# Kernel optimization log

Hardware: AMD Instinct MI355X
Metric: run time of the kernel (lower is better)

## Reference

```python
import jax, jax.numpy as jnp
import numpy as np

EPS = 1e-5
KS = 3
PAD = 1


def _bn(x, g, b, m, v):
    inv = g / jnp.sqrt(v + EPS)
    return x * inv[None, :, None, None] + (b - m * inv)[None, :, None, None]


def _deform_conv2d(x, off_w, off_b, w):
    # x: (B,C,H,W); off_w: (2*9,C,3,3); w: (Cout,C,3,3)
    B, C, H, W = x.shape
    N = KS * KS
    off = jax.lax.conv_general_dilated(x, off_w, (1, 1), ((PAD, PAD), (PAD, PAD)))
    off = off + off_b[None, :, None, None]                      # (B,2N,H,W)
    xp = jnp.pad(x, ((0, 0), (0, 0), (PAD, PAD), (PAD, PAD)))
    Hp, Wp = H + 2 * PAD, W + 2 * PAD
    r = jnp.arange(KS, dtype=x.dtype) - (KS - 1) // 2           # kernel offsets
    pny = jnp.repeat(r, KS)                                     # row-major (dy)
    pnx = jnp.tile(r, KS)                                       # row-major (dx)
    p0y = jnp.arange(1, H + 1, dtype=x.dtype)[None, None, :, None]
    p0x = jnp.arange(1, W + 1, dtype=x.dtype)[None, None, None, :]
    py = off[:, :N] + pny[None, :, None, None] + p0y            # (B,N,H,W)
    px = off[:, N:] + pnx[None, :, None, None] + p0x
    py = jnp.clip(py, 0.0, Hp - 1.0)
    px = jnp.clip(px, 0.0, Wp - 1.0)
    fy = jax.lax.stop_gradient(jnp.floor(py))                   # indices detached (as in torch impl)
    fx = jax.lax.stop_gradient(jnp.floor(px))
    qy0 = jnp.clip(fy, 0.0, Hp - 1.0)
    qx0 = jnp.clip(fx, 0.0, Wp - 1.0)
    qy1 = jnp.clip(fy + 1.0, 0.0, Hp - 1.0)
    qx1 = jnp.clip(fx + 1.0, 0.0, Wp - 1.0)
    xf = xp.reshape(B, C, Hp * Wp)

    def gather(qy, qx):
        idx = (qy * Wp + qx).astype(jnp.int32)                  # (B,N,H,W)
        return jax.vmap(lambda m_, i_: m_[:, i_])(xf, idx)       # (B,C,N,H,W)

    g_lt = (1.0 + (qy0 - py)) * (1.0 + (qx0 - px))
    g_rb = (1.0 - (qy1 - py)) * (1.0 - (qx1 - px))
    g_lb = (1.0 + (qy0 - py)) * (1.0 - (qx1 - px))
    g_rt = (1.0 - (qy1 - py)) * (1.0 + (qx0 - px))
    xo = (g_lt[:, None] * gather(qy0, qx0) + g_rb[:, None] * gather(qy1, qx1)
          + g_lb[:, None] * gather(qy0, qx1) + g_rt[:, None] * gather(qy1, qx0))
    # (B,C,N,H,W) -> (B,C,H*KS,W*KS): N = (row, col) row-major
    xo = xo.reshape(B, C, KS, KS, H, W).transpose(0, 1, 4, 2, 5, 3).reshape(B, C, H * KS, W * KS)
    return jax.lax.conv_general_dilated(xo, w, (KS, KS), 'VALID')


def _forward(x, dc1_offw, dc1_offb, dc1_w, bn1_g, bn1_b, bn1_m, bn1_v,
             dc2_offw, dc2_offb, dc2_w, bn2_g, bn2_b, bn2_m, bn2_v,
             id_w, id_b, bn3_g, bn3_b, bn3_m, bn3_v):
    h = jax.nn.relu(_bn(_deform_conv2d(x, dc1_offw, dc1_offb, dc1_w), bn1_g, bn1_b, bn1_m, bn1_v))
    h = _bn(_deform_conv2d(h, dc2_offw, dc2_offb, dc2_w), bn2_g, bn2_b, bn2_m, bn2_v)
    idt = jnp.einsum('bchw,oc->bohw', x, id_w[:, :, 0, 0]) + id_b[None, :, None, None]
    idt = _bn(idt, bn3_g, bn3_b, bn3_m, bn3_v)
    return jax.nn.relu(h + idt)


def setup_inputs() -> dict:
    key = jax.random.key(0)
    ks = jax.random.split(key, 16)
    B, Cin, Cout, H, W = 2, 64, 128, 128, 128
    N2 = 2 * KS * KS
    d = {}
    d['x'] = jax.random.normal(ks[0], (B, Cin, H, W), jnp.float32)
    d['dc1_offw'] = jax.random.normal(ks[1], (N2, Cin, KS, KS), jnp.float32) * 0.01
    d['dc1_offb'] = jnp.zeros((N2,), jnp.float32)
    d['dc1_w'] = jax.random.normal(ks[2], (Cout, Cin, KS, KS), jnp.float32) * 0.05
    d['bn1_g'] = 1.0 + 0.1 * jax.random.normal(ks[3], (Cout,), jnp.float32)
    d['bn1_b'] = 0.1 * jax.random.normal(ks[4], (Cout,), jnp.float32)
    d['bn1_m'] = 0.1 * jax.random.normal(ks[5], (Cout,), jnp.float32)
    d['bn1_v'] = jnp.ones((Cout,), jnp.float32)
    d['dc2_offw'] = jax.random.normal(ks[6], (N2, Cout, KS, KS), jnp.float32) * 0.01
    d['dc2_offb'] = jnp.zeros((N2,), jnp.float32)
    d['dc2_w'] = jax.random.normal(ks[7], (Cout, Cout, KS, KS), jnp.float32) * 0.03
    d['bn2_g'] = 1.0 + 0.1 * jax.random.normal(ks[8], (Cout,), jnp.float32)
    d['bn2_b'] = 0.1 * jax.random.normal(ks[9], (Cout,), jnp.float32)
    d['bn2_m'] = 0.1 * jax.random.normal(ks[10], (Cout,), jnp.float32)
    d['bn2_v'] = jnp.ones((Cout,), jnp.float32)
    d['id_w'] = jax.random.normal(ks[11], (Cout, Cin, 1, 1), jnp.float32) * 0.1
    d['id_b'] = jnp.zeros((Cout,), jnp.float32)
    d['bn3_g'] = 1.0 + 0.1 * jax.random.normal(ks[12], (Cout,), jnp.float32)
    d['bn3_b'] = 0.1 * jax.random.normal(ks[13], (Cout,), jnp.float32)
    d['bn3_m'] = 0.1 * jax.random.normal(ks[14], (Cout,), jnp.float32)
    d['bn3_v'] = jnp.ones((Cout,), jnp.float32)
    return d


def reference(x, dc1_offw, dc1_offb, dc1_w, bn1_g, bn1_b, bn1_m, bn1_v,
              dc2_offw, dc2_offb, dc2_w, bn2_g, bn2_b, bn2_m, bn2_v,
              id_w, id_b, bn3_g, bn3_b, bn3_m, bn3_v):
    return _forward(x, dc1_offw, dc1_offb, dc1_w, bn1_g, bn1_b, bn1_m, bn1_v,
                    dc2_offw, dc2_offb, dc2_w, bn2_g, bn2_b, bn2_m, bn2_v,
                    id_w, id_b, bn3_g, bn3_b, bn3_m, bn3_v)
```

## Files before the change

kernel.cpp:

```cpp
#include <hip/hip_runtime.h>
#include <math.h>

#define HH 128
#define WW 128
#define HWSZ (HH * WW)
#define BB 2
#define COUT 128

typedef __bf16 bf16x8 __attribute__((ext_vector_type(8)));
typedef float f32x4 __attribute__((ext_vector_type(4)));
typedef float f32x2 __attribute__((ext_vector_type(2)));
typedef short s16x8 __attribute__((ext_vector_type(8)));
typedef short s16x4 __attribute__((ext_vector_type(4)));
typedef unsigned short u16x4 __attribute__((ext_vector_type(4)));
typedef unsigned short u16x8 __attribute__((ext_vector_type(8)));

__device__ __forceinline__ short tobf(float f) {
  union { float f; unsigned u; } v; v.f = f;
  unsigned r = v.u + 0x7fffu + ((v.u >> 16) & 1u);
  return (short)(r >> 16);
}
__device__ __forceinline__ float asf(unsigned u) {
  union { unsigned u; float f; } v; v.u = u;
  return v.f;
}
__device__ __forceinline__ f32x2 up2(unsigned u) {
  f32x2 r; r[0] = asf(u << 16); r[1] = asf(u & 0xffff0000u); return r;
}
__device__ __forceinline__ unsigned trunc2bf(f32x2 v) {
  union { float f; unsigned u; } a, b;
  a.f = v[0]; b.f = v[1];
  return __builtin_amdgcn_perm(b.u, a.u, 0x07060302u);
}

#define PA0 73728
#define PA1 221184
#define PA2 229376
#define PA3 247808
#define PA4 284672
#define PA5 284928
__global__ __launch_bounds__(256) void prep_all_kernel(
    const float* __restrict__ dc1_w, const float* __restrict__ dc2_w,
    const float* __restrict__ id_w, const float* __restrict__ dc1_offw,
    const float* __restrict__ dc2_offw,
    const float* g1, const float* b1, const float* m1, const float* v1,
    const float* g2, const float* b2, const float* m2, const float* v2,
    const float* g3, const float* b3, const float* m3, const float* v3,
    const float* idb,
    short* __restrict__ wbf1, short* __restrict__ wbf2,
    short* __restrict__ woff1, short* __restrict__ woff2,
    float* __restrict__ cb1, float* __restrict__ cb2) {
  int idx = blockIdx.x * 256 + threadIdx.x;
  if (idx < PA0) {
    int o = idx / 576, k = idx - o * 576;
    float inv = g1[o] / sqrtf(v1[o] + 1e-5f);
    int col = (k % 9) * 64 + k / 9;
    int di = (((col >> 5) * 2 + (o >> 6)) * 4 + ((o >> 4) & 3)) * 512
           + (((o & 15) | (((col >> 3) & 3) << 4)) * 8) + (col & 7);
    wbf1[di] = tobf(dc1_w[(size_t)o * 576 + k] * inv);
  } else if (idx < PA1) {
    int j = idx - PA0;
    int o = j / 1152, k = j - o * 1152;
    float inv = g2[o] / sqrtf(v2[o] + 1e-5f);
    int col = (k % 9) * 128 + k / 9;
    int di = (((col >> 5) * 2 + (o >> 6)) * 4 + ((o >> 4) & 3)) * 512
           + (((o & 15) | (((col >> 3) & 3) << 4)) * 8) + (col & 7);
    wbf2[di] = tobf(dc2_w[(size_t)o * 1152 + k] * inv);
  } else if (idx < PA2) {
    int j = idx - PA1;
    int o = j >> 6, k = j & 63;
    float inv = g3[o] / sqrtf(v3[o] + 1e-5f);
    int col = 1152 + k;
    int di = (((col >> 5) * 2 + (o >> 6)) * 4 + ((o >> 4) & 3)) * 512
           + (((o & 15) | (((col >> 3) & 3) << 4)) * 8) + (col & 7);
    wbf2[di] = tobf(id_w[(size_t)o * 64 + k] * inv);
  } else if (idx < PA3) {
    int j = idx - PA2;
    int o = j / 576, k = j - o * 576;
    int col = (k % 9) * 64 + k / 9;
    int di = ((col >> 5) * 2 + (o >> 4)) * 512 + ((col >> 3) & 3) * 128
           + (o & 15) * 8 + (col & 7);
    woff1[di] = (o < 18) ? tobf(dc1_offw[(size_t)o * 576 + k]) : (short)0;
  } else if (idx < PA4) {
    int j = idx - PA3;
    int o = j / 1152, k = j - o * 1152;
    int col = (k % 9) * 128 + k / 9;
    int di = ((col >> 5) * 2 + (o >> 4)) * 512 + ((col >> 3) & 3) * 128
           + (o & 15) * 8 + (col & 7);
    woff2[di] = (o < 18) ? tobf(dc2_offw[(size_t)o * 1152 + k]) : (short)0;
  } else if (idx < PA5) {
    int j = idx - PA4;
    if (j < 128) {
      float inv = g1[j] / sqrtf(v1[j] + 1e-5f);
      cb1[j] = b1[j] - m1[j] * inv;
    } else {
      int o = j - 128;
      float inv2_ = g2[o] / sqrtf(v2[o] + 1e-5f);
      float inv3_ = g3[o] / sqrtf(v3[o] + 1e-5f);
      cb2[o] = (b2[o] - m2[o] * inv2_) + idb[o] * inv3_ + (b3[o] - m3[o] * inv3_);
    }
  }
}

__global__ __launch_bounds__(256) void xcast_kernel(const float* __restrict__ x,
                                                    unsigned short* __restrict__ xn) {
  __shared__ short lds[64 * 72];
  int tid = threadIdx.x;
  int gp0 = blockIdx.x * 64;
  int b = gp0 >> 14;
  int pl0 = gp0 & 16383;
  int p = tid & 63;
  int cb = (tid >> 6) * 16;
#pragma unroll
  for (int i = 0; i < 16; i++) {
    int c = cb + i;
    lds[p * 72 + c] = tobf(x[((size_t)(b * 64 + c)) * HWSZ + pl0 + p]);
  }
  __syncthreads();
  int pw = tid >> 2, cseg = (tid & 3) * 16;
  u16x8 a = *(const u16x8*)&lds[pw * 72 + cseg];
  u16x8 b8 = *(const u16x8*)&lds[pw * 72 + cseg + 8];
  *(u16x8*)&xn[(size_t)(gp0 + pw) * 64 + cseg] = a;
  *(u16x8*)&xn[(size_t)(gp0 + pw) * 64 + cseg + 8] = b8;
}

__global__ __launch_bounds__(512, 4) void offconv_mfma_kernel(
    const unsigned short* __restrict__ in, const short* __restrict__ woff,
    const float* __restrict__ offb, float* __restrict__ off, int cshift) {
  __shared__ float redf[4 * 64 * 8];
  const int tid = threadIdx.x;
  const int lane = tid & 63, wv = tid >> 6;
  const int pxg = wv & 3, kh = wv >> 2;
  const int pb = ((blockIdx.x & 7) << 6) | (blockIdx.x >> 3);
  const int pix0 = pb << 6;
  const int x0 = pix0 & 127, y = (pix0 >> 7) & 127, b = pix0 >> 14;
  const int Cin = 1 << cshift;
  const int HK = (9 << cshift) >> 1;
  const int NCh = HK >> 5;
  const unsigned short* inb = in + (size_t)b * HWSZ * Cin;
  const int l15 = lane & 15, quad = lane >> 4;
  const int px = x0 + pxg * 16 + l15;

  f32x4 acc[2];
  acc[0] = (f32x4){0.f, 0.f, 0.f, 0.f};
  acc[1] = (f32x4){0.f, 0.f, 0.f, 0.f};

  for (int i = 0; i < NCh; i++) {
    int k0 = kh * HK + i * 32;
    int n = k0 >> cshift;
    int c0 = (k0 & (Cin - 1)) + quad * 8;
    int yy = y + n / 3 - 1;
    int xx = px + n % 3 - 1;
    bf16x8 bv = {};
    if (((unsigned)yy < (unsigned)HH) && ((unsigned)xx < (unsigned)WW))
      bv = *(const bf16x8*)&inb[((size_t)yy * WW + xx) * Cin + c0];
    int fbase = (k0 >> 5) * 1024 + lane * 8;
    bf16x8 a0 = *(const bf16x8*)&woff[fbase];
    bf16x8 a1 = *(const bf16x8*)&woff[fbase + 512];
    acc[0] = __builtin_amdgcn_mfma_f32_16x16x32_bf16(a0, bv, acc[0], 0, 0, 0);
    acc[1] = __builtin_amdgcn_mfma_f32_16x16x32_bf16(a1, bv, acc[1], 0, 0, 0);
  }
  if (kh == 1) {
    *(f32x4*)&redf[(pxg * 64 + lane) * 8] = acc[0];
    *(f32x4*)&redf[(pxg * 64 + lane) * 8 + 4] = acc[1];
  }
  __syncthreads();
  if (kh == 0) {
    acc[0] += *(const f32x4*)&redf[(pxg * 64 + lane) * 8];
    acc[1] += *(const f32x4*)&redf[(pxg * 64 + lane) * 8 + 4];
#pragma unroll
    for (int ot = 0; ot < 2; ot++) {
#pragma unroll
      for (int r = 0; r < 4; r++) {
        int o = ot * 16 + quad * 4 + r;
        if (o < 18)
          off[(size_t)(b * 18 + o) * HWSZ + y * WW + px] = acc[ot][r] + offb[o];
      }
    }
  }
}

template <int CSH, int KCONV, int KTOT, int MODE>
__global__ __launch_bounds__(256, 3) void deform_mfma_kernel(
    const unsigned short* __restrict__ in, const float* __restrict__ off,
    const short* __restrict__ wbf, const float* __restrict__ cbv,
    const unsigned short* __restrict__ xid, float* __restrict__ outf,
    unsigned short* __restrict__ outb) {
  __shared__ __align__(16) char smem[25088];
  uint4* dsu = (uint4*)smem;
  f32x4* redf = (f32x4*)smem;
  short* trans = (short*)(smem + 16384);

  const int tid = threadIdx.x;
  const int lane = tid & 63, wv = tid >> 6;
  const int pb = ((blockIdx.x & 7) << 7) | (blockIdx.x >> 3);
  const int pix0 = pb << 5;
  const int x0 = pix0 & 127, y = (pix0 >> 7) & 127, b = pix0 >> 14;
  const int Cin = 1 << CSH;
  const unsigned short* inb = in + (size_t)b * HWSZ * Cin;
  const int l15 = lane & 15, quad = lane >> 4;
  const int pxg = wv & 1, kh = wv >> 1;
  const int dp = pxg * 16 + (lane >> 2);
  const int cq = lane & 3;
  const int baddr = (((lane & 15) << 2) | (lane >> 4)) << 2;

  for (int t = tid; t < 288; t += 256) {
    int n = t >> 5, pp = t & 31;
    float offy = off[(size_t)(b * 18 + n) * HWSZ + y * WW + x0 + pp];
    float offx = off[(size_t)(b * 18 + 9 + n) * HWSZ + y * WW + x0 + pp];
    float py = offy + (float)(n / 3 - 1) + (float)(y + 1);
    float px = offx + (float)(n % 3 - 1) + (float)(x0 + pp + 1);
    py = fminf(fmaxf(py, 0.f), 129.f);
    px = fminf(fmaxf(px, 0.f), 129.f);
    float fy = floorf(py), fx = floorf(px);
    float qy1 = fminf(fy + 1.f, 129.f), qx1 = fminf(fx + 1.f, 129.f);
    float ty0 = 1.f + fy - py, ty1 = 1.f - (qy1 - py);
    float tx0 = 1.f + fx - px, tx1 = 1.f - (qx1 - px);
    int iy0 = (int)fy - 1, ix0 = (int)fx - 1;
    int iy1 = (int)qy1 - 1, ix1 = (int)qx1 - 1;
    if ((unsigned)iy0 >= (unsigned)HH) ty0 = 0.f;
    if ((unsigned)iy1 >= (unsigned)HH) ty1 = 0.f;
    if ((unsigned)ix0 >= (unsigned)WW) tx0 = 0.f;
    if ((unsigned)ix1 >= (unsigned)WW) tx1 = 0.f;
    int by0 = min(max(iy0, 0), HH - 1), by1 = min(max(iy1, 0), HH - 1);
    int bx0 = min(max(ix0, 0), WW - 1), bx1 = min(max(ix1, 0), WW - 1);
    uint4 d4;
    d4.x = (unsigned)(unsigned short)tobf(ty0 * tx0)
         | ((unsigned)(unsigned short)tobf(ty0 * tx1) << 16);
    d4.y = (unsigned)(unsigned short)tobf(ty1 * tx0)
         | ((unsigned)(unsigned short)tobf(ty1 * tx1) << 16);
    d4.z = (unsigned)((by0 * WW + bx0) * Cin);
    d4.w = (unsigned)((((by1 - by0) * WW * Cin) << 16) | ((bx1 - bx0) * Cin));
    dsu[t] = d4;
  }

  f32x4 acc[8];
#pragma unroll
  for (int j = 0; j < 8; j++) acc[j] = (f32x4){0.f, 0.f, 0.f, 0.f};

  __syncthreads();

  constexpr int NC = KTOT >> 5;
  constexpr int HC = NC >> 1;
  const short* wfb = wbf + lane * 8;

  for (int i = 0; i < HC; i++) {
    int kc = kh * HC + i;
    int k0 = kc << 5;
    const short* wf = wfb + (size_t)kc * 4096;
    bf16x8 a0 = *(const bf16x8*)(wf);
    bf16x8 a1 = *(const bf16x8*)(wf + 512);
    bf16x8 a2 = *(const bf16x8*)(wf + 1024);
    bf16x8 a3 = *(const bf16x8*)(wf + 1536);
    bf16x8 a4 = *(const bf16x8*)(wf + 2048);
    bf16x8 a5 = *(const bf16x8*)(wf + 2560);
    bf16x8 a6 = *(const bf16x8*)(wf + 3072);
    bf16x8 a7 = *(const bf16x8*)(wf + 3584);
    uint4 pk;
    if (k0 < KCONV) {
      int n = k0 >> CSH;
      int c0 = (k0 & (Cin - 1)) + cq * 8;
      uint4 d4 = dsu[(n << 5) + dp];
      int dx = (int)(d4.w & 0xffffu);
      int dy = (int)d4.w >> 16;
      const unsigned short* ptr = inb + (int)d4.z + c0;
      uint4 q00 = *(const uint4*)(ptr);
      uint4 q01 = *(const uint4*)(ptr + dx);
      uint4 q10 = *(const uint4*)(ptr + dy);
      uint4 q11 = *(const uint4*)(ptr + dx + dy);
      float w0 = asf(d4.x << 16), w1 = asf(d4.x & 0xffff0000u);
      float w2 = asf(d4.y << 16), w3 = asf(d4.y & 0xffff0000u);
      f32x2 v0 = up2(q00.x) * w0 + up2(q01.x) * w1 + up2(q10.x) * w2 + up2(q11.x) * w3;
      f32x2 v1 = up2(q00.y) * w0 + up2(q01.y) * w1 + up2(q10.y) * w2 + up2(q11.y) * w3;
      f32x2 v2 = up2(q00.z) * w0 + up2(q01.z) * w1 + up2(q10.z) * w2 + up2(q11.z) * w3;
      f32x2 v3 = up2(q00.w) * w0 + up2(q01.w) * w1 + up2(q10.w) * w2 + up2(q11.w) * w3;
      pk.x = trunc2bf(v0); pk.y = trunc2bf(v1);
      pk.z = trunc2bf(v2); pk.w = trunc2bf(v3);
    } else {
      int c = (k0 - KCONV) + cq * 8;
      pk = *(const uint4*)&xid[((size_t)(b * HWSZ) + y * WW + x0 + dp) * 64 + c];
    }
    union { int i[4]; bf16x8 v; } bu;
    bu.i[0] = __builtin_amdgcn_ds_bpermute(baddr, (int)pk.x);
    bu.i[1] = __builtin_amdgcn_ds_bpermute(baddr, (int)pk.y);
    bu.i[2] = __builtin_amdgcn_ds_bpermute(baddr, (int)pk.z);
    bu.i[3] = __builtin_amdgcn_ds_bpermute(baddr, (int)pk.w);
    bf16x8 bfr = bu.v;
    acc[0] = __builtin_amdgcn_mfma_f32_16x16x32_bf16(a0, bfr, acc[0], 0, 0, 0);
    acc[1] = __builtin_amdgcn_mfma_f32_16x16x32_bf16(a1, bfr, acc[1], 0, 0, 0);
    acc[2] = __builtin_amdgcn_mfma_f32_16x16x32_bf16(a2, bfr, acc[2], 0, 0, 0);
    acc[3] = __builtin_amdgcn_mfma_f32_16x16x32_bf16(a3, bfr, acc[3], 0, 0, 0);
    acc[4] = __builtin_amdgcn_mfma_f32_16x16x32_bf16(a4, bfr, acc[4], 0, 0, 0);
    acc[5] = __builtin_amdgcn_mfma_f32_16x16x32_bf16(a5, bfr, acc[5], 0, 0, 0);
    acc[6] = __builtin_amdgcn_mfma_f32_16x16x32_bf16(a6, bfr, acc[6], 0, 0, 0);
    acc[7] = __builtin_amdgcn_mfma_f32_16x16x32_bf16(a7, bfr, acc[7], 0, 0, 0);
  }

  __syncthreads();
  if (kh == 1) {
#pragma unroll
    for (int f = 0; f < 8; f++) redf[f * 128 + pxg * 64 + lane] = acc[f];
  }
  __syncthreads();
  if (kh == 0) {
#pragma unroll
    for (int f = 0; f < 8; f++) acc[f] += redf[f * 128 + pxg * 64 + lane];
    if (MODE == 1) {
#pragma unroll
      for (int f = 0; f < 8; f++) {
#pragma unroll
        for (int r = 0; r < 4; r++) {
          int o = (f >> 2) * 64 + (f & 3) * 16 + quad * 4 + r;
          outf[(size_t)(b * COUT + o) * HWSZ + y * WW + x0 + pxg * 16 + l15] =
              fmaxf(acc[f][r] + cbv[o], 0.f);
        }
      }
    } else {
      int pl = pxg * 16 + l15;
#pragma unroll
      for (int f = 0; f < 8; f++) {
        s16x4 t4;
#pragma unroll
        for (int r = 0; r < 4; r++) {
          int o = (f >> 2) * 64 + (f & 3) * 16 + quad * 4 + r;
          t4[r] = tobf(fmaxf(acc[f][r] + cbv[o], 0.f));
        }
        *(s16x4*)&trans[pl * 136 + (f >> 2) * 64 + (f & 3) * 16 + quad * 4] = t4;
      }
    }
  }
  if (MODE == 0) {
    __syncthreads();
    int pw = tid >> 3, cs = (tid & 7) * 16;
    u16x8 va = *(const u16x8*)&trans[pw * 136 + cs];
    u16x8 vb = *(const u16x8*)&trans[pw * 136 + cs + 8];
    size_t gb = ((size_t)(b * HWSZ) + y * WW + x0 + pw) * 128 + cs;
    *(u16x8*)&outb[gb] = va;
    *(u16x8*)&outb[gb + 8] = vb;
  }
}

extern "C" void kernel_launch(void* const* d_in, const int* in_sizes, int n_in,
                              void* d_out, int out_size, void* d_ws, size_t ws_size,
                              hipStream_t stream) {
  const float* x        = (const float*)d_in[0];
  const float* dc1_offw = (const float*)d_in[1];
  const float* dc1_offb = (const float*)d_in[2];
  const float* dc1_w    = (const float*)d_in[3];
  const float* bn1_g    = (const float*)d_in[4];
  const float* bn1_b    = (const float*)d_in[5];
  const float* bn1_m    = (const float*)d_in[6];
  const float* bn1_v    = (const float*)d_in[7];
  const float* dc2_offw = (const float*)d_in[8];
  const float* dc2_offb = (const float*)d_in[9];
  const float* dc2_w    = (const float*)d_in[10];
  const float* bn2_g    = (const float*)d_in[11];
  const float* bn2_b    = (const float*)d_in[12];
  const float* bn2_m    = (const float*)d_in[13];
  const float* bn2_v    = (const float*)d_in[14];
  const float* id_w     = (const float*)d_in[15];
  const float* id_b     = (const float*)d_in[16];
  const float* bn3_g    = (const float*)d_in[17];
  const float* bn3_b    = (const float*)d_in[18];
  const float* bn3_m    = (const float*)d_in[19];
  const float* bn3_v    = (const float*)d_in[20];

  float* wsf = (float*)d_ws;
  float* off1 = wsf;
  float* off2 = off1 + (size_t)BB * 18 * HWSZ;
  float* cb1  = off2 + (size_t)BB * 18 * HWSZ;
  float* cb2  = cb1 + 128;
  unsigned short* xbf = (unsigned short*)(cb2 + 128);
  unsigned short* h1  = xbf + (size_t)BB * HWSZ * 64;
  short* wbf1  = (short*)(h1 + (size_t)BB * HWSZ * COUT);
  short* wbf2  = wbf1 + (size_t)128 * 576;
  short* woff1 = wbf2 + (size_t)128 * 1216;
  short* woff2 = woff1 + (size_t)18 * 1024;

  hipLaunchKernelGGL(prep_all_kernel, dim3((PA5 + 255) / 256), dim3(256), 0, stream,
                     dc1_w, dc2_w, id_w, dc1_offw, dc2_offw,
                     bn1_g, bn1_b, bn1_m, bn1_v, bn2_g, bn2_b, bn2_m, bn2_v,
                     bn3_g, bn3_b, bn3_m, bn3_v, id_b,
                     wbf1, wbf2, woff1, woff2, cb1, cb2);
  hipLaunchKernelGGL(xcast_kernel, dim3(BB * HWSZ / 64), dim3(256), 0, stream, x, xbf);

  hipLaunchKernelGGL(offconv_mfma_kernel, dim3(512), dim3(512), 0, stream,
                     xbf, woff1, dc1_offb, off1, 6);
  hipLaunchKernelGGL((deform_mfma_kernel<6, 576, 576, 0>), dim3(1024), dim3(256), 0, stream,
                     xbf, off1, wbf1, cb1, (const unsigned short*)nullptr,
                     (float*)nullptr, h1);
  hipLaunchKernelGGL(offconv_mfma_kernel, dim3(512), dim3(512), 0, stream,
                     h1, woff2, dc2_offb, off2, 7);
  hipLaunchKernelGGL((deform_mfma_kernel<7, 1152, 1216, 1>), dim3(1024), dim3(256), 0, stream,
                     h1, off2, wbf2, cb2, xbf, (float*)d_out,
                     (unsigned short*)nullptr);
}
```

Measured before the change: 187.5 us.

## Software-pipeline deform conv gathers with double-buffered registers; template offset conv

The deform kernel's K loop now double-buffers weight fragments and bilinear gather loads in two register sets (A/B), so the loads for the next chunk are issued before the current chunk's interpolation and MFMAs run. The conv part and the identity part are split into separate loops, which removes the per-iteration branch. The offset conv kernel is templated on the channel shift so its loop count is a compile-time constant and can be fully unrolled. The extra register sets raise VGPR pressure under launch_bounds(256,3), which risks spills or lower occupancy.

```diff
diff --git a/kernel.cpp b/kernel.cpp
--- a/kernel.cpp
+++ b/kernel.cpp
@@ -124,19 +124,20 @@
   *(u16x8*)&xn[(size_t)(gp0 + pw) * 64 + cseg + 8] = b8;
 }
 
+template <int CSH>
 __global__ __launch_bounds__(512, 4) void offconv_mfma_kernel(
     const unsigned short* __restrict__ in, const short* __restrict__ woff,
-    const float* __restrict__ offb, float* __restrict__ off, int cshift) {
+    const float* __restrict__ offb, float* __restrict__ off) {
   __shared__ float redf[4 * 64 * 8];
+  constexpr int Cin = 1 << CSH;
+  constexpr int HK = (9 << CSH) >> 1;
+  constexpr int NCh = HK >> 5;
   const int tid = threadIdx.x;
   const int lane = tid & 63, wv = tid >> 6;
   const int pxg = wv & 3, kh = wv >> 2;
   const int pb = ((blockIdx.x & 7) << 6) | (blockIdx.x >> 3);
   const int pix0 = pb << 6;
   const int x0 = pix0 & 127, y = (pix0 >> 7) & 127, b = pix0 >> 14;
-  const int Cin = 1 << cshift;
-  const int HK = (9 << cshift) >> 1;
-  const int NCh = HK >> 5;
   const unsigned short* inb = in + (size_t)b * HWSZ * Cin;
   const int l15 = lane & 15, quad = lane >> 4;
   const int px = x0 + pxg * 16 + l15;
@@ -145,9 +146,10 @@
   acc[0] = (f32x4){0.f, 0.f, 0.f, 0.f};
   acc[1] = (f32x4){0.f, 0.f, 0.f, 0.f};
 
+#pragma unroll
   for (int i = 0; i < NCh; i++) {
     int k0 = kh * HK + i * 32;
-    int n = k0 >> cshift;
+    int n = k0 >> CSH;
     int c0 = (k0 & (Cin - 1)) + quad * 8;
     int yy = y + n / 3 - 1;
     int xx = px + n % 3 - 1;
@@ -180,6 +182,64 @@
   }
 }
 
+#define LOADW(P, kc_)                                           \
+  {                                                             \
+    const short* wf_ = wfb + (size_t)(kc_) * 4096;              \
+    P##w0 = *(const bf16x8*)(wf_);                              \
+    P##w1 = *(const bf16x8*)(wf_ + 512);                        \
+    P##w2 = *(const bf16x8*)(wf_ + 1024);                       \
+    P##w3 = *(const bf16x8*)(wf_ + 1536);                       \
+    P##w4 = *(const bf16x8*)(wf_ + 2048);                       \
+    P##w5 = *(const bf16x8*)(wf_ + 2560);                       \
+    P##w6 = *(const bf16x8*)(wf_ + 3072);                       \
+    P##w7 = *(const bf16x8*)(wf_ + 3584);                       \
+  }
+
+#define LOADT(P, kc_)                                           \
+  {                                                             \
+    int k0_ = (kc_) << 5;                                       \
+    int n_ = k0_ >> CSH;                                        \
+    int c0_ = (k0_ & (Cin - 1)) + cq * 8;                       \
+    uint4 d4_ = dsu[(n_ << 5) + dp];                            \
+    int dx_ = (int)(d4_.w & 0xffffu);                           \
+    int dy_ = (int)d4_.w >> 16;                                 \
+    const unsigned short* ptr_ = inb + (int)d4_.z + c0_;        \
+    P##q0 = *(const uint4*)(ptr_);                              \
+    P##q1 = *(const uint4*)(ptr_ + dx_);                        \
+    P##q2 = *(const uint4*)(ptr_ + dy_);                        \
+    P##q3 = *(const uint4*)(ptr_ + dx_ + dy_);                  \
+    P##wa = d4_.x;                                              \
+    P##wb = d4_.y;                                              \
+  }
+
+#define COMPUTE(P)                                                            \
+  {                                                                           \
+    float w0_ = asf(P##wa << 16), w1_ = asf(P##wa & 0xffff0000u);             \
+    float w2_ = asf(P##wb << 16), w3_ = asf(P##wb & 0xffff0000u);             \
+    f32x2 v0_ = up2(P##q0.x) * w0_ + up2(P##q1.x) * w1_                       \
+              + up2(P##q2.x) * w2_ + up2(P##q3.x) * w3_;                      \
+    f32x2 v1_ = up2(P##q0.y) * w0_ + up2(P##q1.y) * w1_                       \
+              + up2(P##q2.y) * w2_ + up2(P##q3.y) * w3_;                      \
+    f32x2 v2_ = up2(P##q0.z) * w0_ + up2(P##q1.z) * w1_                       \
+              + up2(P##q2.z) * w2_ + up2(P##q3.z) * w3_;                      \
+    f32x2 v3_ = up2(P##q0.w) * w0_ + up2(P##q1.w) * w1_                       \
+              + up2(P##q2.w) * w2_ + up2(P##q3.w) * w3_;                      \
+    union { int i[4]; bf16x8 v; } bu_;                                        \
+    bu_.i[0] = __builtin_amdgcn_ds_bpermute(baddr, (int)trunc2bf(v0_));       \
+    bu_.i[1] = __builtin_amdgcn_ds_bpermute(baddr, (int)trunc2bf(v1_));       \
+    bu_.i[2] = __builtin_amdgcn_ds_bpermute(baddr, (int)trunc2bf(v2_));       \
+    bu_.i[3] = __builtin_amdgcn_ds_bpermute(baddr, (int)trunc2bf(v3_));       \
+    bf16x8 bfr_ = bu_.v;                                                      \
+    acc[0] = __builtin_amdgcn_mfma_f32_16x16x32_bf16(P##w0, bfr_, acc[0], 0, 0, 0); \
+    acc[1] = __builtin_amdgcn_mfma_f32_16x16x32_bf16(P##w1, bfr_, acc[1], 0, 0, 0); \
+    acc[2] = __builtin_amdgcn_mfma_f32_16x16x32_bf16(P##w2, bfr_, acc[2], 0, 0, 0); \
+    acc[3] = __builtin_amdgcn_mfma_f32_16x16x32_bf16(P##w3, bfr_, acc[3], 0, 0, 0); \
+    acc[4] = __builtin_amdgcn_mfma_f32_16x16x32_bf16(P##w4, bfr_, acc[4], 0, 0, 0); \
+    acc[5] = __builtin_amdgcn_mfma_f32_16x16x32_bf16(P##w5, bfr_, acc[5], 0, 0, 0); \
+    acc[6] = __builtin_amdgcn_mfma_f32_16x16x32_bf16(P##w6, bfr_, acc[6], 0, 0, 0); \
+    acc[7] = __builtin_amdgcn_mfma_f32_16x16x32_bf16(P##w7, bfr_, acc[7], 0, 0, 0); \
+  }
+
 template <int CSH, int KCONV, int KTOT, int MODE>
 __global__ __launch_bounds__(256, 3) void deform_mfma_kernel(
     const unsigned short* __restrict__ in, const float* __restrict__ off,
@@ -196,13 +256,28 @@
   const int pb = ((blockIdx.x & 7) << 7) | (blockIdx.x >> 3);
   const int pix0 = pb << 5;
   const int x0 = pix0 & 127, y = (pix0 >> 7) & 127, b = pix0 >> 14;
-  const int Cin = 1 << CSH;
+  constexpr int Cin = 1 << CSH;
   const unsigned short* inb = in + (size_t)b * HWSZ * Cin;
   const int l15 = lane & 15, quad = lane >> 4;
   const int pxg = wv & 1, kh = wv >> 1;
   const int dp = pxg * 16 + (lane >> 2);
   const int cq = lane & 3;
   const int baddr = (((lane & 15) << 2) | (lane >> 4)) << 2;
+
+  constexpr int NC = KTOT >> 5;
+  constexpr int NCONV = KCONV >> 5;
+  constexpr int HC = NC >> 1;
+  const int kcBeg = kh * HC;
+  const int kcEnd = kcBeg + HC;
+  const int kcEndConv = (kcEnd < NCONV) ? kcEnd : NCONV;
+  const short* wfb = wbf + lane * 8;
+
+  bf16x8 Aw0, Aw1, Aw2, Aw3, Aw4, Aw5, Aw6, Aw7;
+  bf16x8 Bw0, Bw1, Bw2, Bw3, Bw4, Bw5, Bw6, Bw7;
+  uint4 Aq0, Aq1, Aq2, Aq3, Bq0, Bq1, Bq2, Bq3;
+  unsigned Awa, Awb, Bwa, Bwb;
+
+  LOADW(A, kcBeg);
 
   for (int t = tid; t < 288; t += 256) {
     int n = t >> 5, pp = t & 31;
@@ -240,60 +315,43 @@
 
   __syncthreads();
 
-  constexpr int NC = KTOT >> 5;
-  constexpr int HC = NC >> 1;
-  const short* wfb = wbf + lane * 8;
-
-  for (int i = 0; i < HC; i++) {
-    int kc = kh * HC + i;
-    int k0 = kc << 5;
-    const short* wf = wfb + (size_t)kc * 4096;
-    bf16x8 a0 = *(const bf16x8*)(wf);
-    bf16x8 a1 = *(const bf16x8*)(wf + 512);
-    bf16x8 a2 = *(const bf16x8*)(wf + 1024);
-    bf16x8 a3 = *(const bf16x8*)(wf + 1536);
-    bf16x8 a4 = *(const bf16x8*)(wf + 2048);
-    bf16x8 a5 = *(const bf16x8*)(wf + 2560);
-    bf16x8 a6 = *(const bf16x8*)(wf + 3072);
-    bf16x8 a7 = *(const bf16x8*)(wf + 3584);
-    uint4 pk;
-    if (k0 < KCONV) {
-      int n = k0 >> CSH;
-      int c0 = (k0 & (Cin - 1)) + cq * 8;
-      uint4 d4 = dsu[(n << 5) + dp];
-      int dx = (int)(d4.w & 0xffffu);
-      int dy = (int)d4.w >> 16;
-      const unsigned short* ptr = inb + (int)d4.z + c0;
-      uint4 q00 = *(const uint4*)(ptr);
-      uint4 q01 = *(const uint4*)(ptr + dx);
-      uint4 q10 = *(const uint4*)(ptr + dy);
-      uint4 q11 = *(const uint4*)(ptr + dx + dy);
-      float w0 = asf(d4.x << 16), w1 = asf(d4.x & 0xffff0000u);
-      float w2 = asf(d4.y << 16), w3 = asf(d4.y & 0xffff0000u);
-      f32x2 v0 = up2(q00.x) * w0 + up2(q01.x) * w1 + up2(q10.x) * w2 + up2(q11.x) * w3;
-      f32x2 v1 = up2(q00.y) * w0 + up2(q01.y) * w1 + up2(q10.y) * w2 + up2(q11.y) * w3;
-      f32x2 v2 = up2(q00.z) * w0 + up2(q01.z) * w1 + up2(q10.z) * w2 + up2(q11.z) * w3;
-      f32x2 v3 = up2(q00.w) * w0 + up2(q01.w) * w1 + up2(q10.w) * w2 + up2(q11.w) * w3;
-      pk.x = trunc2bf(v0); pk.y = trunc2bf(v1);
-      pk.z = trunc2bf(v2); pk.w = trunc2bf(v3);
-    } else {
-      int c = (k0 - KCONV) + cq * 8;
-      pk = *(const uint4*)&xid[((size_t)(b * HWSZ) + y * WW + x0 + dp) * 64 + c];
+  LOADT(A, kcBeg);
+  int i = kcBeg;
+  for (; i + 2 <= kcEndConv; i += 2) {
+    LOADW(B, i + 1);
+    LOADT(B, i + 1);
+    COMPUTE(A);
+    if (i + 2 < kcEndConv) {
+      LOADW(A, i + 2);
+      LOADT(A, i + 2);
     }
-    union { int i[4]; bf16x8 v; } bu;
-    bu.i[0] = __builtin_amdgcn_ds_bpermute(baddr, (int)pk.x);
-    bu.i[1] = __builtin_amdgcn_ds_bpermute(baddr, (int)pk.y);
-    bu.i[2] = __builtin_amdgcn_ds_bpermute(baddr, (int)pk.z);
-    bu.i[3] = __builtin_amdgcn_ds_bpermute(baddr, (int)pk.w);
-    bf16x8 bfr = bu.v;
-    acc[0] = __builtin_amdgcn_mfma_f32_16x16x32_bf16(a0, bfr, acc[0], 0, 0, 0);
-    acc[1] = __builtin_amdgcn_mfma_f32_16x16x32_bf16(a1, bfr, acc[1], 0, 0, 0);
-    acc[2] = __builtin_amdgcn_mfma_f32_16x16x32_bf16(a2, bfr, acc[2], 0, 0, 0);
-    acc[3] = __builtin_amdgcn_mfma_f32_16x16x32_bf16(a3, bfr, acc[3], 0, 0, 0);
-    acc[4] = __builtin_amdgcn_mfma_f32_16x16x32_bf16(a4, bfr, acc[4], 0, 0, 0);
-    acc[5] = __builtin_amdgcn_mfma_f32_16x16x32_bf16(a5, bfr, acc[5], 0, 0, 0);
-    acc[6] = __builtin_amdgcn_mfma_f32_16x16x32_bf16(a6, bfr, acc[6], 0, 0, 0);
-    acc[7] = __builtin_amdgcn_mfma_f32_16x16x32_bf16(a7, bfr, acc[7], 0, 0, 0);
+    COMPUTE(B);
+  }
+  if (i < kcEndConv) {
+    COMPUTE(A);
+    i++;
+  }
+
+  if (KCONV < KTOT) {
+    for (; i < kcEnd; i++) {
+      LOADW(A, i);
+      int c = ((i << 5) - KCONV) + cq * 8;
+      uint4 pk = *(const uint4*)&xid[((size_t)(b * HWSZ) + y * WW + x0 + dp) * 64 + c];
+      union { int i[4]; bf16x8 v; } bu;
+      bu.i[0] = __builtin_amdgcn_ds_bpermute(baddr, (int)pk.x);
+      bu.i[1] = __builtin_amdgcn_ds_bpermute(baddr, (int)pk.y);
+      bu.i[2] = __builtin_amdgcn_ds_bpermute(baddr, (int)pk.z);
+      bu.i[3] = __builtin_amdgcn_ds_bpermute(baddr, (int)pk.w);
+      bf16x8 bfr = bu.v;
+      acc[0] = __builtin_amdgcn_mfma_f32_16x16x32_bf16(Aw0, bfr, acc[0], 0, 0, 0);
+      acc[1] = __builtin_amdgcn_mfma_f32_16x16x32_bf16(Aw1, bfr, acc[1], 0, 0, 0);
+      acc[2] = __builtin_amdgcn_mfma_f32_16x16x32_bf16(Aw2, bfr, acc[2], 0, 0, 0);
+      acc[3] = __builtin_amdgcn_mfma_f32_16x16x32_bf16(Aw3, bfr, acc[3], 0, 0, 0);
+      acc[4] = __builtin_amdgcn_mfma_f32_16x16x32_bf16(Aw4, bfr, acc[4], 0, 0, 0);
+      acc[5] = __builtin_amdgcn_mfma_f32_16x16x32_bf16(Aw5, bfr, acc[5], 0, 0, 0);
+      acc[6] = __builtin_amdgcn_mfma_f32_16x16x32_bf16(Aw6, bfr, acc[6], 0, 0, 0);
+      acc[7] = __builtin_amdgcn_mfma_f32_16x16x32_bf16(Aw7, bfr, acc[7], 0, 0, 0);
+    }
   }
 
   __syncthreads();
@@ -384,13 +442,13 @@
                      wbf1, wbf2, woff1, woff2, cb1, cb2);
   hipLaunchKernelGGL(xcast_kernel, dim3(BB * HWSZ / 64), dim3(256), 0, stream, x, xbf);
 
-  hipLaunchKernelGGL(offconv_mfma_kernel, dim3(512), dim3(512), 0, stream,
-                     xbf, woff1, dc1_offb, off1, 6);
+  hipLaunchKernelGGL((offconv_mfma_kernel<6>), dim3(512), dim3(512), 0, stream,
+                     xbf, woff1, dc1_offb, off1);
   hipLaunchKernelGGL((deform_mfma_kernel<6, 576, 576, 0>), dim3(1024), dim3(256), 0, stream,
                      xbf, off1, wbf1, cb1, (const unsigned short*)nullptr,
                      (float*)nullptr, h1);
-  hipLaunchKernelGGL(offconv_mfma_kernel, dim3(512), dim3(512), 0, stream,
-                     h1, woff2, dc2_offb, off2, 7);
+  hipLaunchKernelGGL((offconv_mfma_kernel<7>), dim3(512), dim3(512), 0, stream,
+                     h1, woff2, dc2_offb, off2);
   hipLaunchKernelGGL((deform_mfma_kernel<7, 1152, 1216, 1>), dim3(1024), dim3(256), 0, stream,
                      h1, off2, wbf2, cb2, xbf, (float*)d_out,
                      (unsigned short*)nullptr);
```

Measured after the change: 182.5 us. -2.7%, faster.
